# Optimization experiments

Hardware: AMD Instinct MI355X
Metric: run time of the kernel (lower is better)

## Reference

```python
import jax, jax.numpy as jnp
import numpy as np

TOP_K = 2
SCALING = 32.0 / 16.0  # lora_alpha / r

N, D, O = 4096, 4096, 4096   # tokens, in_features, out_features
E, H, R_RANK = 8, 3, 16      # experts, B-heads per expert, lora rank
W_SCALE = 0.02               # keep logits in a sane range


def setup_inputs() -> dict:
    key = jax.random.key(0)
    ks = jax.random.split(key, 6)
    return {
        "x": jax.random.normal(ks[0], (N, D), jnp.float32),
        "base_W": jax.random.normal(ks[1], (D, O), jnp.float32) * W_SCALE,
        "router_W": jax.random.normal(ks[2], (E, D), jnp.float32) * W_SCALE,
        "A": jax.random.normal(ks[3], (E, D, R_RANK), jnp.float32) * W_SCALE,
        "B": jax.random.normal(ks[4], (E, H, R_RANK, O), jnp.float32) * W_SCALE,
        "R": jax.random.normal(ks[5], (E, D, H), jnp.float32) * W_SCALE,
    }


def reference(x, base_W, router_W, A, B, R):
    # Base dense layer
    base = x @ base_W                                   # [N, O]
    # Expert router: softmax over experts, top-k gate renormalized
    probs = jax.nn.softmax(x @ router_W.T, axis=-1)     # [N, E]
    topv, topi = jax.lax.top_k(probs, TOP_K)            # [N, k]
    topv = topv / topv.sum(-1, keepdims=True)
    n_idx = jnp.arange(x.shape[0])[:, None]
    gate = jnp.zeros_like(probs).at[n_idx, topi].set(topv)  # dense [N, E] gate, 0 off top-k
    # Shared lora_A per expert
    a = jnp.einsum('nd,edr->ner', x, A)                 # [N, E, r]
    # Per-expert head router over lora_B heads
    head_w = jax.nn.softmax(jnp.einsum('nd,edh->neh', x, R), axis=-1)  # [N, E, H]
    # Head-weighted B projections, combined with expert gates
    delta = jnp.einsum('ner,neh,ehro,ne->no', a, head_w, B, gate)      # [N, O]
    return base + SCALING * delta
```

## Files before the change

kernel.cpp:

```cpp
#include <hip/hip_runtime.h>
#include <hip/hip_bf16.h>
#include <math.h>

typedef __bf16 bf16_t;
typedef __bf16 bf16x4_t __attribute__((ext_vector_type(4)));
typedef __bf16 bf16x8_t __attribute__((ext_vector_type(8)));
typedef float  f32x4_t  __attribute__((ext_vector_type(4)));

#define N_TOK 4096
#define D_IN  4096
#define O_OUT 4096
#define NEXP  8
#define NHEAD 3
#define RANK  16
#define KC2   384
#define PCOLS 256
#define NKZ   8
#define SCALING_F 2.0f


__device__ __forceinline__ void transpose_tile(const float* __restrict__ src,
                                               bf16_t* __restrict__ dst,
                                               int Rr, int Cc, int r0, int c0,
                                               float (*tile)[65]) {
  int q  = threadIdx.x & 15;
  int r4 = threadIdx.x >> 4;
  #pragma unroll
  for (int g = 0; g < 4; ++g) {
    int r = r4 + g * 16;
    float4 v = *(const float4*)(src + (size_t)(r0 + r) * Cc + c0 + q * 4);
    tile[r][q * 4 + 0] = v.x; tile[r][q * 4 + 1] = v.y;
    tile[r][q * 4 + 2] = v.z; tile[r][q * 4 + 3] = v.w;
  }
  __syncthreads();
  int j  = threadIdx.x & 7;
  int cc = threadIdx.x >> 3;
  #pragma unroll
  for (int h = 0; h < 2; ++h) {
    int c = cc + h * 32;
    bf16x8_t o;
    #pragma unroll
    for (int i = 0; i < 8; ++i) o[i] = (bf16_t)tile[j * 8 + i][c];
    *(bf16x8_t*)(dst + (size_t)(c0 + c) * Rr + r0 + j * 8) = o;
  }
}

__global__ __launch_bounds__(256) void prep_kernel(const float* __restrict__ x,
                                                   const float* __restrict__ base_W,
                                                   const float* __restrict__ rw,
                                                   const float* __restrict__ A,
                                                   const float* __restrict__ B,
                                                   const float* __restrict__ Rm,
                                                   bf16_t* __restrict__ xb,
                                                   bf16_t* __restrict__ WbT,
                                                   bf16_t* __restrict__ BbT,
                                                   bf16_t* __restrict__ PabT,
                                                   int* __restrict__ gidx,
                                                   float* __restrict__ gwv) {
  __shared__ float tile[64][65];
  int b = blockIdx.x;
  if (b < 4096) {
    transpose_tile(base_W, WbT, 4096, 4096, (b & 63) * 64, (b >> 6) * 64, tile);
  } else if (b < 5120) {
    int lane = threadIdx.x & 63;
    int wv = threadIdx.x >> 6;
    int n = (b - 4096) * 4 + wv;
    const float4* xv = (const float4*)(x + (size_t)n * D_IN);
    bf16x4_t* xo = (bf16x4_t*)(xb + (size_t)n * D_IN);
    float acc[NEXP] = {0, 0, 0, 0, 0, 0, 0, 0};
    for (int d = lane; d < D_IN / 4; d += 64) {
      float4 xx = xv[d];
      bf16x4_t ob = { (bf16_t)xx.x, (bf16_t)xx.y, (bf16_t)xx.z, (bf16_t)xx.w };
      xo[d] = ob;
      #pragma unroll
      for (int e = 0; e < NEXP; ++e) {
        float4 ww = ((const float4*)(rw + (size_t)e * D_IN))[d];
        acc[e] += xx.x * ww.x + xx.y * ww.y + xx.z * ww.z + xx.w * ww.w;
      }
    }
    #pragma unroll
    for (int e = 0; e < NEXP; ++e) {
      float v = acc[e];
      #pragma unroll
      for (int o = 32; o > 0; o >>= 1) v += __shfl_down(v, o);
      acc[e] = v;
    }
    if (lane == 0) {
      int i0 = 0; float l0 = acc[0];
      #pragma unroll
      for (int e = 1; e < NEXP; ++e) if (acc[e] > l0) { l0 = acc[e]; i0 = e; }
      int i1 = -1; float l1 = -3.4e38f;
      #pragma unroll
      for (int e = 0; e < NEXP; ++e) if (e != i0 && acc[e] > l1) { l1 = acc[e]; i1 = e; }
      float w0 = 1.f / (1.f + expf(l1 - l0));
      gidx[2 * n] = i0; gidx[2 * n + 1] = i1;
      gwv[2 * n] = w0;  gwv[2 * n + 1] = 1.f - w0;
    }
  } else if (b < 5504) {
    int t = b - 5120;
    transpose_tile(B, BbT, KC2, 4096, (t % 6) * 64, (t / 6) * 64, tile);
  } else {
    int c = b - 5504;
    for (int d = threadIdx.x; d < D_IN; d += 256) {
      float v = 0.f;
      if (c < 128) {
        int e = c >> 4, r = c & 15;
        v = A[((size_t)e * D_IN + d) * RANK + r];
      } else if (c < 152) {
        int qq = c - 128; int e = qq / 3, h = qq - 3 * e;
        v = Rm[((size_t)e * D_IN + d) * NHEAD + h];
      }
      PabT[(size_t)c * D_IN + d] = (bf16_t)v;
    }
  }
}

__global__ void gating_kernel(const float* __restrict__ projP, const int* __restrict__ gidx,
                              const float* __restrict__ gwv, bf16_t* __restrict__ C2b) {
  int n = blockIdx.x;
  int c = threadIdx.x;
  int e = c / 48;
  int h = (c % 48) / 16;
  int r = c & 15;
  int i0 = gidx[2 * n], i1 = gidx[2 * n + 1];
  float g = (e == i0) ? gwv[2 * n] : (e == i1) ? gwv[2 * n + 1] : 0.f;
  float val = 0.f;
  if (g != 0.f) {
    const float* p0 = projP + (size_t)n * PCOLS;
    const size_t S = (size_t)N_TOK * PCOLS;
    float h0 = 0.f, h1 = 0.f, h2 = 0.f, av = 0.f;
    #pragma unroll
    for (int z = 0; z < NKZ; ++z) {
      const float* pz = p0 + (size_t)z * S;
      h0 += pz[128 + e * 3 + 0];
      h1 += pz[128 + e * 3 + 1];
      h2 += pz[128 + e * 3 + 2];
      av += pz[e * 16 + r];
    }
    float mx = fmaxf(h0, fmaxf(h1, h2));
    float e0 = expf(h0 - mx), e1 = expf(h1 - mx), e2 = expf(h2 - mx);
    float hw = (h == 0 ? e0 : h == 1 ? e1 : e2) / (e0 + e1 + e2);
    val = SCALING_F * g * hw * av;
  }
  C2b[(size_t)n * KC2 + c] = (bf16_t)val;
}

__device__ __forceinline__ void run_kloop(f32x4_t (&acc)[4][4], bf16_t* sA, bf16_t* sB,
                                          const bf16_t* __restrict__ Ab, int lda,
                                          const bf16_t* __restrict__ Bb, int ldb, int K) {
  const int tid = threadIdx.x;
  const int lane = tid & 63;
  const int w = tid >> 6;
  const int wm = (w >> 1) * 64;
  const int wn = (w & 1) * 64;
  const int qd = lane >> 4;
  const int ln = lane & 15;
  const int sw = ln & 7;

  size_t offA[4], offB[4];
  int lo[4];
  #pragma unroll
  for (int t = 0; t < 4; ++t) {
    int c = tid + t * 256;
    int m = c >> 3, kc = (c & 7) ^ (m & 7);
    offA[t] = (size_t)m * lda + kc * 8;
    offB[t] = (size_t)m * ldb + kc * 8;
    lo[t] = c * 8;
  }
  int rowA[4], rowB[4];
  #pragma unroll
  for (int i = 0; i < 4; ++i) {
    rowA[i] = (wm + i * 16 + ln) * 64;
    rowB[i] = (wn + i * 16 + ln) * 64;
  }

  for (int k0 = 0; k0 < K; k0 += 64) {
    __syncthreads();
    #pragma unroll
    for (int t = 0; t < 4; ++t)
      __builtin_amdgcn_global_load_lds(
          (const __attribute__((address_space(1))) void*)(Ab + k0 + offA[t]),
          (__attribute__((address_space(3))) void*)(sA + lo[t]), 16, 0, 0);
    #pragma unroll
    for (int t = 0; t < 4; ++t)
      __builtin_amdgcn_global_load_lds(
          (const __attribute__((address_space(1))) void*)(Bb + k0 + offB[t]),
          (__attribute__((address_space(3))) void*)(sB + lo[t]), 16, 0, 0);
    __syncthreads();
    #pragma unroll
    for (int s = 0; s < 2; ++s) {
      bf16x8_t af[4], bfr[4];
      int kx = ((s * 4 + qd) ^ sw) * 8;
      #pragma unroll
      for (int i = 0; i < 4; ++i) af[i]  = *(const bf16x8_t*)(sA + rowA[i] + kx);
      #pragma unroll
      for (int i = 0; i < 4; ++i) bfr[i] = *(const bf16x8_t*)(sB + rowB[i] + kx);
      #pragma unroll
      for (int i = 0; i < 4; ++i)
        #pragma unroll
        for (int j = 0; j < 4; ++j)
          acc[i][j] = __builtin_amdgcn_mfma_f32_16x16x32_bf16(af[i], bfr[j], acc[i][j], 0, 0, 0);
    }
  }
}

__global__ __launch_bounds__(256) void gemm_proj_kernel(const bf16_t* __restrict__ xb,
                                                        const bf16_t* __restrict__ PabT,
                                                        float* __restrict__ projP) {
  __shared__ bf16_t sA[128 * 64];
  __shared__ bf16_t sB[128 * 64];
  int bm = blockIdx.x, bn = blockIdx.y, kz = blockIdx.z;
  f32x4_t acc[4][4] = {};
  run_kloop(acc, sA, sB,
            xb + (size_t)bm * 128 * D_IN + kz * 512, D_IN,
            PabT + (size_t)bn * 128 * D_IN + kz * 512, D_IN, 512);
  const int lane = threadIdx.x & 63, w = threadIdx.x >> 6;
  const int wm = (w >> 1) * 64, wn = (w & 1) * 64, qd = lane >> 4, ln = lane & 15;
  float* Cb = projP + (size_t)kz * N_TOK * PCOLS + (size_t)bm * 128 * PCOLS + bn * 128;
  #pragma unroll
  for (int i = 0; i < 4; ++i)
    #pragma unroll
    for (int j = 0; j < 4; ++j) {
      int col = wn + j * 16 + ln;
      #pragma unroll
      for (int rg = 0; rg < 4; ++rg) {
        int row = wm + i * 16 + qd * 4 + rg;
        Cb[(size_t)row * PCOLS + col] = acc[i][j][rg];
      }
    }
}


__device__ __forceinline__ void stage2(const bf16_t* __restrict__ G, int k0,
                                       bf16_t* lbase, size_t g0, size_t g1, int tid) {
  __builtin_amdgcn_global_load_lds(
      (const __attribute__((address_space(1))) void*)(G + g0 + k0),
      (__attribute__((address_space(3))) void*)(lbase + tid * 8), 16, 0, 0);
  __builtin_amdgcn_global_load_lds(
      (const __attribute__((address_space(1))) void*)(G + g1 + k0),
      (__attribute__((address_space(3))) void*)(lbase + 4096 + tid * 8), 16, 0, 0);
}

template <int N>
__device__ __forceinline__ void vm_wait() {
  if constexpr (N == 8)      asm volatile("s_waitcnt vmcnt(8)" ::: "memory");
  else if constexpr (N == 4) asm volatile("s_waitcnt vmcnt(4)" ::: "memory");
  else if constexpr (N == 0) asm volatile("s_waitcnt vmcnt(0)" ::: "memory");
}

template <int MB>
__device__ __forceinline__ void mfma16(f32x4_t (&acc)[8][4], const bf16x8_t (&af)[4],
                                       const bf16x8_t (&bv)[4]) {
  __builtin_amdgcn_s_setprio(1);
  #pragma unroll
  for (int mi = 0; mi < 4; ++mi)
    #pragma unroll
    for (int nj = 0; nj < 4; ++nj)
      acc[MB + mi][nj] =
          __builtin_amdgcn_mfma_f32_16x16x32_bf16(af[mi], bv[nj], acc[MB + mi][nj], 0, 0, 0);
  __builtin_amdgcn_s_setprio(0);
}

template <int SC, bool STAGE, int VMN, bool NEXTRD>
__device__ __forceinline__ void tbodyP(f32x4_t (&acc)[8][4], bf16_t* sring,
                                       const bf16_t* __restrict__ Ag,
                                       const bf16_t* __restrict__ Bg, int k3,
                                       size_t gA0, size_t gA1, size_t gB0, size_t gB1,
                                       int aoff, int boff, int tid,
                                       bf16x8_t (&bv)[4], bf16x8_t (&a0)[4]) {
  constexpr int SS = (SC + 3) & 3;
  constexpr int SN = (SC + 1) & 3;
  if constexpr (STAGE) stage2(Ag, k3, sring + SS * 16384, gA0, gA1, tid);
  const bf16_t* pA = sring + SC * 16384 + aoff;
  bf16x8_t a1[4];
  mfma16<0>(acc, a0, bv);
  #pragma unroll
  for (int mi = 0; mi < 4; ++mi) a1[mi] = *(const bf16x8_t*)(pA + (4 + mi) * 512);
  if constexpr (STAGE) stage2(Bg, k3, sring + SS * 16384 + 8192, gB0, gB1, tid);
  vm_wait<VMN>();
  __builtin_amdgcn_s_barrier();
  mfma16<4>(acc, a1, bv);
  if constexpr (NEXTRD) {
    const bf16_t* qA = sring + SN * 16384 + aoff;
    const bf16_t* qB = sring + SN * 16384 + 8192 + boff;
    #pragma unroll
    for (int nj = 0; nj < 4; ++nj) bv[nj] = *(const bf16x8_t*)(qB + nj * 512);
    #pragma unroll
    for (int mi = 0; mi < 4; ++mi) a0[mi] = *(const bf16x8_t*)(qA + mi * 512);
  }
  __builtin_amdgcn_sched_barrier(0);
  __builtin_amdgcn_s_barrier();
}

template <int K>
__device__ __forceinline__ void kloopP(f32x4_t (&acc)[8][4], bf16_t* sring,
                                       const bf16_t* __restrict__ A, int lda,
                                       const bf16_t* __restrict__ B, int ldb,
                                       int tid, int aoff, int boff) {
  constexpr int T = K / 32;
  static_assert((T & 3) == 0, "T must be multiple of 4");
  const int s0 = tid,       r0 = s0 >> 2, c0 = (s0 & 3) ^ ((r0 >> 1) & 3);
  const int s1 = 512 + tid, r1 = s1 >> 2, c1 = (s1 & 3) ^ ((r1 >> 1) & 3);
  const size_t gA0 = (size_t)r0 * lda + c0 * 8, gA1 = (size_t)r1 * lda + c1 * 8;
  const size_t gB0 = (size_t)r0 * ldb + c0 * 8, gB1 = (size_t)r1 * ldb + c1 * 8;

  #pragma unroll
  for (int t = 0; t < 3; ++t) {
    stage2(A, t * 32, sring + t * 16384, gA0, gA1, tid);
    stage2(B, t * 32, sring + t * 16384 + 8192, gB0, gB1, tid);
  }
  asm volatile("s_waitcnt vmcnt(8)" ::: "memory");
  __builtin_amdgcn_s_barrier();
  bf16x8_t bv[4], a0[4];
  {
    const bf16_t* qA = sring + aoff;
    const bf16_t* qB = sring + 8192 + boff;
    #pragma unroll
    for (int nj = 0; nj < 4; ++nj) bv[nj] = *(const bf16x8_t*)(qB + nj * 512);
    #pragma unroll
    for (int mi = 0; mi < 4; ++mi) a0[mi] = *(const bf16x8_t*)(qA + mi * 512);
  }
  constexpr int TM = T - 3;
  int t = 0;
  for (; t + 3 < TM; t += 4) {
    tbodyP<0,true,8,true>(acc, sring, A, B, (t+3)*32, gA0,gA1,gB0,gB1, aoff,boff,tid, bv,a0);
    tbodyP<1,true,8,true>(acc, sring, A, B, (t+4)*32, gA0,gA1,gB0,gB1, aoff,boff,tid, bv,a0);
    tbodyP<2,true,8,true>(acc, sring, A, B, (t+5)*32, gA0,gA1,gB0,gB1, aoff,boff,tid, bv,a0);
    tbodyP<3,true,8,true>(acc, sring, A, B, (t+6)*32, gA0,gA1,gB0,gB1, aoff,boff,tid, bv,a0);
  }
  tbodyP<0,true,8,true>(acc, sring, A, B, (t+3)*32, gA0,gA1,gB0,gB1, aoff,boff,tid, bv,a0);
  tbodyP<1,false,4,true >(acc, sring, A, B, 0, gA0,gA1,gB0,gB1, aoff,boff,tid, bv,a0);
  tbodyP<2,false,0,true >(acc, sring, A, B, 0, gA0,gA1,gB0,gB1, aoff,boff,tid, bv,a0);
  tbodyP<3,false,-1,false>(acc, sring, A, B, 0, gA0,gA1,gB0,gB1, aoff,boff,tid, bv,a0);
}

__global__ __launch_bounds__(512, 1) void gemm_fused256(const bf16_t* __restrict__ xb,
                                                        const bf16_t* __restrict__ WbT,
                                                        const bf16_t* __restrict__ C2b,
                                                        const bf16_t* __restrict__ BbT,
                                                        float* __restrict__ out) {
  __shared__ __align__(16) bf16_t sring[4 * 16384];
  const int tid = threadIdx.x;
  const int lane = tid & 63;
  const int w = tid >> 6;
  const int wm = w >> 2;
  const int wn = w & 3;
  const int qd = lane >> 4;
  const int ln = lane & 15;
  const int swz8 = ((qd ^ ((ln >> 1) & 3)) << 3);

  int b = blockIdx.x;
  int sw = (b & 7) * 32 + (b >> 3);
  int bm = sw >> 4, bn = sw & 15;

  const int aoff = (wm * 128 + ln) * 32 + swz8;
  const int boff = (wn * 64 + ln) * 32 + swz8;

  f32x4_t acc[8][4] = {};

  kloopP<D_IN>(acc, sring, xb  + (size_t)bm * 256 * D_IN, D_IN,
                           WbT + (size_t)bn * 256 * D_IN, D_IN, tid, aoff, boff);
  kloopP<KC2>(acc, sring, C2b + (size_t)bm * 256 * KC2,  KC2,
                          BbT + (size_t)bn * 256 * KC2,  KC2,  tid, aoff, boff);

  float* Cb = out + (size_t)(bm * 256 + wm * 128) * O_OUT + bn * 256 + wn * 64;
  #pragma unroll
  for (int mi = 0; mi < 8; ++mi)
    #pragma unroll
    for (int nj = 0; nj < 4; ++nj)
      #pragma unroll
      for (int rg = 0; rg < 4; ++rg)
        Cb[(size_t)(mi * 16 + qd * 4 + rg) * O_OUT + nj * 16 + ln] = acc[mi][nj][rg];
}

extern "C" void kernel_launch(void* const* d_in, const int* in_sizes, int n_in,
                              void* d_out, int out_size, void* d_ws, size_t ws_size,
                              hipStream_t stream) {
  const float* x       = (const float*)d_in[0];
  const float* base_W  = (const float*)d_in[1];
  const float* routerW = (const float*)d_in[2];
  const float* A       = (const float*)d_in[3];
  const float* B       = (const float*)d_in[4];
  const float* Rm      = (const float*)d_in[5];
  float* out = (float*)d_out;
  char* ws = (char*)d_ws;

  bf16_t* xb   = (bf16_t*)(ws);
  bf16_t* WbT  = (bf16_t*)(ws + 33554432);
  bf16_t* PabT = (bf16_t*)(ws + 67108864);
  bf16_t* BbT  = (bf16_t*)(ws + 69206016);
  bf16_t* C2b  = (bf16_t*)(ws + 72351744);
  int*    gidx = (int*)   (ws + 75497472);
  float*  gwv  = (float*) (ws + 75530240);
  float*  projP = out;

  prep_kernel<<<5760, 256, 0, stream>>>(x, base_W, routerW, A, B, Rm,
                                        xb, WbT, BbT, PabT, gidx, gwv);
  gemm_proj_kernel<<<dim3(32, 2, NKZ), 256, 0, stream>>>(xb, PabT, projP);
  gating_kernel<<<4096, 384, 0, stream>>>(projP, gidx, gwv, C2b);
  gemm_fused256<<<dim3(256), 512, 0, stream>>>(xb, WbT, C2b, BbT, out);
}
```

Before: 348.0 us.

## Merge projection GEMM and gating into one kernel with grid barrier

Fuses the split-K projection GEMM and the gating kernel into one 512-block launch. An atomic-counter grid barrier, reset in prep_kernel, separates the two phases, and the gating work becomes a grid-stride loop. This removes one kernel launch and its drain/fill gap. It relies on all 512 blocks being co-resident, or the barrier deadlocks. Separately, the main GEMM pipeline body is reordered so the second MFMA group is issued before the vmcnt wait and barrier, with the trailing barrier removed. This is meant to overlap math with load waits.

```diff
diff --git a/kernel.cpp b/kernel.cpp
--- a/kernel.cpp
+++ b/kernel.cpp
@@ -56,9 +56,11 @@
                                                    bf16_t* __restrict__ BbT,
                                                    bf16_t* __restrict__ PabT,
                                                    int* __restrict__ gidx,
-                                                   float* __restrict__ gwv) {
+                                                   float* __restrict__ gwv,
+                                                   unsigned* __restrict__ bar) {
   __shared__ float tile[64][65];
   int b = blockIdx.x;
+  if (b == 0 && threadIdx.x == 0) *bar = 0u;
   if (b < 4096) {
     transpose_tile(base_W, WbT, 4096, 4096, (b & 63) * 64, (b >> 6) * 64, tile);
   } else if (b < 5120) {
@@ -115,36 +117,6 @@
   }
 }
 
-__global__ void gating_kernel(const float* __restrict__ projP, const int* __restrict__ gidx,
-                              const float* __restrict__ gwv, bf16_t* __restrict__ C2b) {
-  int n = blockIdx.x;
-  int c = threadIdx.x;
-  int e = c / 48;
-  int h = (c % 48) / 16;
-  int r = c & 15;
-  int i0 = gidx[2 * n], i1 = gidx[2 * n + 1];
-  float g = (e == i0) ? gwv[2 * n] : (e == i1) ? gwv[2 * n + 1] : 0.f;
-  float val = 0.f;
-  if (g != 0.f) {
-    const float* p0 = projP + (size_t)n * PCOLS;
-    const size_t S = (size_t)N_TOK * PCOLS;
-    float h0 = 0.f, h1 = 0.f, h2 = 0.f, av = 0.f;
-    #pragma unroll
-    for (int z = 0; z < NKZ; ++z) {
-      const float* pz = p0 + (size_t)z * S;
-      h0 += pz[128 + e * 3 + 0];
-      h1 += pz[128 + e * 3 + 1];
-      h2 += pz[128 + e * 3 + 2];
-      av += pz[e * 16 + r];
-    }
-    float mx = fmaxf(h0, fmaxf(h1, h2));
-    float e0 = expf(h0 - mx), e1 = expf(h1 - mx), e2 = expf(h2 - mx);
-    float hw = (h == 0 ? e0 : h == 1 ? e1 : e2) / (e0 + e1 + e2);
-    val = SCALING_F * g * hw * av;
-  }
-  C2b[(size_t)n * KC2 + c] = (bf16_t)val;
-}
-
 __device__ __forceinline__ void run_kloop(f32x4_t (&acc)[4][4], bf16_t* sA, bf16_t* sB,
                                           const bf16_t* __restrict__ Ab, int lda,
                                           const bf16_t* __restrict__ Bb, int ldb, int K) {
@@ -204,30 +176,83 @@
   }
 }
 
-__global__ __launch_bounds__(256) void gemm_proj_kernel(const bf16_t* __restrict__ xb,
-                                                        const bf16_t* __restrict__ PabT,
-                                                        float* __restrict__ projP) {
+__device__ __forceinline__ void grid_sync(unsigned* bar) {
+  __syncthreads();
+  if (threadIdx.x == 0) {
+    __threadfence();
+    unsigned arrived = atomicAdd(bar, 1u) + 1u;
+    if (arrived < 512u) {
+      while (__hip_atomic_load(bar, __ATOMIC_RELAXED, __HIP_MEMORY_SCOPE_AGENT) < 512u) {
+        __builtin_amdgcn_s_sleep(8);
+      }
+    }
+    __threadfence();
+  }
+  __syncthreads();
+}
+
+__global__ __launch_bounds__(256, 2) void proj_gating_kernel(const bf16_t* __restrict__ xb,
+                                                             const bf16_t* __restrict__ PabT,
+                                                             float* __restrict__ projP,
+                                                             const int* __restrict__ gidx,
+                                                             const float* __restrict__ gwv,
+                                                             bf16_t* __restrict__ C2b,
+                                                             unsigned* __restrict__ bar) {
   __shared__ bf16_t sA[128 * 64];
   __shared__ bf16_t sB[128 * 64];
-  int bm = blockIdx.x, bn = blockIdx.y, kz = blockIdx.z;
-  f32x4_t acc[4][4] = {};
-  run_kloop(acc, sA, sB,
-            xb + (size_t)bm * 128 * D_IN + kz * 512, D_IN,
-            PabT + (size_t)bn * 128 * D_IN + kz * 512, D_IN, 512);
-  const int lane = threadIdx.x & 63, w = threadIdx.x >> 6;
-  const int wm = (w >> 1) * 64, wn = (w & 1) * 64, qd = lane >> 4, ln = lane & 15;
-  float* Cb = projP + (size_t)kz * N_TOK * PCOLS + (size_t)bm * 128 * PCOLS + bn * 128;
-  #pragma unroll
-  for (int i = 0; i < 4; ++i)
-    #pragma unroll
-    for (int j = 0; j < 4; ++j) {
-      int col = wn + j * 16 + ln;
-      #pragma unroll
-      for (int rg = 0; rg < 4; ++rg) {
-        int row = wm + i * 16 + qd * 4 + rg;
-        Cb[(size_t)row * PCOLS + col] = acc[i][j][rg];
+  const int lin = blockIdx.x;
+  const int bm = lin & 31, bn = (lin >> 5) & 1, kz = lin >> 6;
+  {
+    f32x4_t acc[4][4] = {};
+    run_kloop(acc, sA, sB,
+              xb + (size_t)bm * 128 * D_IN + kz * 512, D_IN,
+              PabT + (size_t)bn * 128 * D_IN + kz * 512, D_IN, 512);
+    const int lane = threadIdx.x & 63, w = threadIdx.x >> 6;
+    const int wm = (w >> 1) * 64, wn = (w & 1) * 64, qd = lane >> 4, ln = lane & 15;
+    float* Cb = projP + (size_t)kz * N_TOK * PCOLS + (size_t)bm * 128 * PCOLS + bn * 128;
+    #pragma unroll
+    for (int i = 0; i < 4; ++i)
+      #pragma unroll
+      for (int j = 0; j < 4; ++j) {
+        int col = wn + j * 16 + ln;
+        #pragma unroll
+        for (int rg = 0; rg < 4; ++rg) {
+          int row = wm + i * 16 + qd * 4 + rg;
+          Cb[(size_t)row * PCOLS + col] = acc[i][j][rg];
+        }
       }
-    }
+  }
+  grid_sync(bar);
+  const unsigned NTOT = (unsigned)N_TOK * KC2;
+  for (unsigned idx = (unsigned)blockIdx.x * 256u + threadIdx.x; idx < NTOT;
+       idx += 512u * 256u) {
+    int n = (int)(idx / (unsigned)KC2);
+    int c = (int)(idx - (unsigned)n * KC2);
+    int e = c / 48;
+    int h = (c % 48) / 16;
+    int r = c & 15;
+    int i0 = gidx[2 * n], i1 = gidx[2 * n + 1];
+    float g = (e == i0) ? gwv[2 * n] : (e == i1) ? gwv[2 * n + 1] : 0.f;
+    float val = 0.f;
+    if (g != 0.f) {
+      const float* p0 = projP + (size_t)n * PCOLS;
+      const size_t S = (size_t)N_TOK * PCOLS;
+      float h0 = 0.f, h1 = 0.f, h2 = 0.f, av = 0.f;
+      #pragma unroll
+      for (int z = 0; z < NKZ; ++z) {
+        const float* pz = p0 + (size_t)z * S;
+        h0 += pz[128 + e * 3 + 0];
+        h1 += pz[128 + e * 3 + 1];
+        h2 += pz[128 + e * 3 + 2];
+        av += pz[e * 16 + r];
+      }
+      float mx = fmaxf(h0, fmaxf(h1, h2));
+      float e0 = expf(h0 - mx), e1 = expf(h1 - mx), e2 = expf(h2 - mx);
+      float hw = (h == 0 ? e0 : h == 1 ? e1 : e2) / (e0 + e1 + e2);
+      val = SCALING_F * g * hw * av;
+    }
+    C2b[(size_t)n * KC2 + c] = (bf16_t)val;
+  }
 }
 
 
@@ -277,9 +302,11 @@
   #pragma unroll
   for (int mi = 0; mi < 4; ++mi) a1[mi] = *(const bf16x8_t*)(pA + (4 + mi) * 512);
   if constexpr (STAGE) stage2(Bg, k3, sring + SS * 16384 + 8192, gB0, gB1, tid);
+  mfma16<4>(acc, a1, bv);
   vm_wait<VMN>();
+  __builtin_amdgcn_sched_barrier(0);
   __builtin_amdgcn_s_barrier();
-  mfma16<4>(acc, a1, bv);
+  __builtin_amdgcn_sched_barrier(0);
   if constexpr (NEXTRD) {
     const bf16_t* qA = sring + SN * 16384 + aoff;
     const bf16_t* qB = sring + SN * 16384 + 8192 + boff;
@@ -288,8 +315,6 @@
     #pragma unroll
     for (int mi = 0; mi < 4; ++mi) a0[mi] = *(const bf16x8_t*)(qA + mi * 512);
   }
-  __builtin_amdgcn_sched_barrier(0);
-  __builtin_amdgcn_s_barrier();
 }
 
 template <int K>
@@ -311,6 +336,7 @@
   }
   asm volatile("s_waitcnt vmcnt(8)" ::: "memory");
   __builtin_amdgcn_s_barrier();
+  __builtin_amdgcn_sched_barrier(0);
   bf16x8_t bv[4], a0[4];
   {
     const bf16_t* qA = sring + aoff;
@@ -392,11 +418,11 @@
   bf16_t* C2b  = (bf16_t*)(ws + 72351744);
   int*    gidx = (int*)   (ws + 75497472);
   float*  gwv  = (float*) (ws + 75530240);
+  unsigned* bar = (unsigned*)(ws + 75563008);
   float*  projP = out;
 
   prep_kernel<<<5760, 256, 0, stream>>>(x, base_W, routerW, A, B, Rm,
-                                        xb, WbT, BbT, PabT, gidx, gwv);
-  gemm_proj_kernel<<<dim3(32, 2, NKZ), 256, 0, stream>>>(xb, PabT, projP);
-  gating_kernel<<<4096, 384, 0, stream>>>(projP, gidx, gwv, C2b);
+                                        xb, WbT, BbT, PabT, gidx, gwv, bar);
+  proj_gating_kernel<<<512, 256, 0, stream>>>(xb, PabT, projP, gidx, gwv, C2b, bar);
   gemm_fused256<<<dim3(256), 512, 0, stream>>>(xb, WbT, C2b, BbT, out);
 }
```

Measured after the change: 414.5 us. 19.1% more time.
